# Kernel optimization log

Hardware: AMD Instinct MI355X
Metric: run time of the kernel (lower is better)

## Reference

```python
import jax, jax.numpy as jnp
import numpy as np
from jax import lax

NUM_ROUTES = 3
OUT_CAPS = 8
OUT_CH = 16


def squash(t):
    # squared_norm * t / ((1 + squared_norm) * sqrt(squared_norm)), norm over last dim
    sn = jnp.sum(t * t, axis=-1, keepdims=True)
    return sn * t / ((1.0 + sn) * jnp.sqrt(sn))


def setup_inputs() -> dict:
    key = jax.random.key(0)
    k1, k2 = jax.random.split(key)
    x = jax.random.normal(k1, (16, 8, 16, 128, 128), dtype=jnp.float32)
    # conv weight [out_channels*out_capsules, in_channels, 4, 4], kaiming-ish scale
    W_conv = jax.random.normal(k2, (OUT_CH * OUT_CAPS, 16, 4, 4), dtype=jnp.float32) * 0.05
    b_conv = jnp.zeros((OUT_CH * OUT_CAPS,), dtype=jnp.float32)
    return {"x": x, "W_conv": W_conv, "b_conv": b_conv}


def reference(x, W_conv, b_conv):
    B, IC, Cin, W, H = x.shape
    xr = x.reshape(B * IC, Cin, W, H)
    u = lax.conv_general_dilated(
        xr, W_conv,
        window_strides=(2, 2), padding=((2, 2), (2, 2)),
        dimension_numbers=("NCHW", "OIHW", "NCHW"),
    ) + b_conv[None, :, None, None]
    ow, oh = u.shape[2], u.shape[3]
    # [B*IC, OC*Cout, ow, oh] -> [B, IC, ow, oh, OC, Cout]
    u_hat = u.transpose(0, 2, 3, 1).reshape(B, IC, ow, oh, OUT_CAPS, OUT_CH)

    b_ij = jnp.zeros((1, IC, ow, oh, OUT_CAPS), dtype=u_hat.dtype)
    v_j = None
    for it in range(NUM_ROUTES):
        c_ij = jax.nn.softmax(b_ij, axis=1)[..., None]      # [1,IC,ow,oh,OC,1]
        s_j = jnp.sum(c_ij * u_hat, axis=1)                  # [B,ow,oh,OC,Cout]
        v_j = squash(s_j)
        if it < NUM_ROUTES - 1:
            # agreement: dot over Cout between u_hat and v_j
            a_ij = jnp.einsum('biwhoc,bwhoc->biwho', u_hat, v_j)
            b_ij = b_ij + jnp.mean(a_ij, axis=0, keepdims=True)
    # [B,ow,oh,OC,Cout] -> [B, OC, Cout, ow, oh]
    return v_j.transpose(0, 3, 4, 1, 2)
```

## Files before the change

kernel.cpp:

```cpp
#include <hip/hip_runtime.h>
#include <math.h>

#define BB   16
#define IC   8
#define BI   128
#define CIN  16
#define WH   128
#define OWH  65
#define NPIX (OWH*OWH)
#define OC   8
#define COUT 16
#define NOC  128
#define KTOT 256
#define KC   64
#define NCHUNK 4
#define S_TOTAL (CIN*WH*WH)

#define NCHM 8

typedef unsigned short ushortT;
typedef __bf16 bf16x8 __attribute__((ext_vector_type(8)));
typedef float  f32x4  __attribute__((ext_vector_type(4)));

__device__ __forceinline__ ushortT f2bf(float f) {
    unsigned u = __float_as_uint(f);
    unsigned r = (u + 0x7fffu + ((u >> 16) & 1u)) >> 16;
    return (ushortT)r;
}

template <int CTRL>
__device__ __forceinline__ float dppMov(float x) {
    return __int_as_float(__builtin_amdgcn_update_dpp(
        0, __float_as_int(x), CTRL, 0xF, 0xF, true));
}

#define GEMM_BARRIER() do {                                   \
    asm volatile("s_waitcnt lgkmcnt(0)" ::: "memory");        \
    __builtin_amdgcn_s_barrier();                             \
    __builtin_amdgcn_sched_barrier(0);                        \
} while (0)

__global__ void cvtT_kernel(const float* __restrict__ x,
                            ushortT* __restrict__ xbfT)
{
    __shared__ ushortT tile[64 * 136];
    const int t  = threadIdx.x;
    const int s0 = blockIdx.x * 64;

#pragma unroll
    for (int k = 0; k < 8; ++k) {
        const int j  = t + k * 256;
        const int bi = j >> 4, s4 = j & 15;
        const float4 v = *(const float4*)(x + (size_t)bi * S_TOTAL + s0 + s4 * 4);
        const int si = s4 * 4;
        tile[(si    ) * 136 + (bi ^ (((si    ) & 15) << 3))] = f2bf(v.x);
        tile[(si + 1) * 136 + (bi ^ (((si + 1) & 15) << 3))] = f2bf(v.y);
        tile[(si + 2) * 136 + (bi ^ (((si + 2) & 15) << 3))] = f2bf(v.z);
        tile[(si + 3) * 136 + (bi ^ (((si + 3) & 15) << 3))] = f2bf(v.w);
    }
    __syncthreads();
#pragma unroll
    for (int k = 0; k < 4; ++k) {
        const int j  = t + k * 256;
        const int sI = j >> 4, g = j & 15;
        const uint4 val = *(const uint4*)&tile[sI * 136 + ((g ^ (sI & 15)) << 3)];
        *(uint4*)(xbfT + (size_t)(s0 + sI) * 128 + g * 8) = val;
    }
}

__global__ void prep_w_kernel(const float* __restrict__ W,
                              ushortT* __restrict__ Wbf)
{
    int idx = blockIdx.x * 256 + threadIdx.x;
    int oc = idx >> 8, k = idx & 255;
    int kpg = k >> 3, j = k & 7;
    Wbf[((size_t)kpg * 128 + oc) * 8 + j] = f2bf(W[idx]);
}

__launch_bounds__(512, 4)
__global__ void capsconv_mfma(const ushortT* __restrict__ xbfT,
                              const ushortT* __restrict__ Wbf,
                              const float* __restrict__ bias,
                              float* __restrict__ outbuf,
                              const int direct_out)
{
    __shared__ __align__(16) ushortT As[3][4 * 128 * 8];
    __shared__ float cijs[64];
    __shared__ float bijs[64];
    __shared__ float aTmp[16 * 64];

    const int t  = threadIdx.x;
    const int g8 = blockIdx.x;
    int p = (g8 & 7) * 529 + (g8 >> 3);
    if (p >= NPIX) return;

    const int w  = t >> 6;
    const int ln = t & 63;
    const int q  = ln >> 4;
    const int cL = ln & 15;
    const int h  = q & 1;
    const int mrow_base = 64 * (w >> 2);
    const int ncol_base = 32 * (w & 3);

    const int px = p / OWH;
    const int py = p % OWH;
    const int row0 = 2 * px - 2;
    const int col0 = 2 * py - 2;

    f32x4 acc[4][2];
#pragma unroll
    for (int mt = 0; mt < 4; ++mt)
#pragma unroll
        for (int nt = 0; nt < 2; ++nt) acc[mt][nt] = (f32x4){0.f, 0.f, 0.f, 0.f};

    const int g     = t & 15;
    const int sI    = t >> 4;
    const int colw  = sI & 3;
    const int rowl  = (sI >> 2) & 3;
    const int cih   = sI >> 4;
    const int srow  = row0 + rowl;
    const int scol  = col0 + colw;
    const bool ok   = (srow >= 0 && srow < WH && scol >= 0 && scol < WH);
    const size_t aoff0 = ok
        ? ((size_t)((cih * WH + srow) * WH + scol) * 128 + g * 8)
        : 0;
    const int kpg   = cih * 2 + (rowl >> 1);
    const int jj    = (rowl & 1) * 4 + colw;
    const int wbase = (kpg * 128 + g * 8) * 16 + jj * 2;
    const int gk7   = g & 7;

    int aRd[4];
#pragma unroll
    for (int mt = 0; mt < 4; ++mt) {
        const int by = (q * 128 + mrow_base + mt * 16 + cL) * 16;
        aRd[mt] = by ^ (((by >> 7) & 7) << 4);
    }

    uint4 aR[2];

    auto loadA = [&](uint4& r, int kc) {
        r = make_uint4(0u, 0u, 0u, 0u);
        if (ok) r = *(const uint4*)(xbfT + aoff0 + (size_t)kc * (2 * WH * WH * 128));
    };
    auto storeA = [&](int buf, const uint4& r) {
        char* ab = (char*)&As[buf][0];
        const ushortT* av = (const ushortT*)&r;
#pragma unroll
        for (int c = 0; c < 8; ++c)
            *(ushortT*)(ab + wbase + ((c ^ gk7) << 4)) = av[c];
    };

    loadA(aR[0], 0);
    loadA(aR[1], 1);
    storeA(0, aR[0]);
    loadA(aR[0], 2);
    GEMM_BARRIER();

#pragma unroll
    for (int kc = 0; kc < NCHM; ++kc) {
        const int buf = kc % 3;
        {
            const char* abase = (const char*)&As[buf][0];
            bf16x8 af[4], bfr[2];
#pragma unroll
            for (int mt = 0; mt < 4; ++mt)
                af[mt] = *(const bf16x8*)(abase + aRd[mt]);
            const ushortT* bsrc = Wbf + kc * 4096 + (q * 128 + ncol_base + cL) * 8;
            bfr[0] = *(const bf16x8*)(bsrc);
            bfr[1] = *(const bf16x8*)(bsrc + 128);
#pragma unroll
            for (int mt = 0; mt < 4; ++mt)
#pragma unroll
                for (int nt = 0; nt < 2; ++nt)
                    acc[mt][nt] = __builtin_amdgcn_mfma_f32_16x16x32_bf16(
                        af[mt], bfr[nt], acc[mt][nt], 0, 0, 0);
        }
        if (kc + 1 < NCHM) storeA((kc + 1) % 3, aR[(kc + 1) & 1]);
        if (kc + 3 < NCHM) loadA(aR[(kc + 3) & 1], kc + 3);
        GEMM_BARRIER();
    }

#pragma unroll
    for (int nt = 0; nt < 2; ++nt) {
        const float bv = bias[ncol_base + nt * 16 + cL];
#pragma unroll
        for (int mt = 0; mt < 4; ++mt) acc[mt][nt] += bv;
    }

    for (int it = 0; it < 3; ++it) {
        float4 cf4[2];
        if (it == 0) {
#pragma unroll
            for (int nt = 0; nt < 2; ++nt)
                cf4[nt] = make_float4(0.125f, 0.125f, 0.125f, 0.125f);
        } else {
#pragma unroll
            for (int nt = 0; nt < 2; ++nt)
                cf4[nt] = *(const float4*)&cijs[(2 * (w & 3) + nt) * 8 + 4 * h];
        }

#pragma unroll
        for (int mt = 0; mt < 4; ++mt) {
            const int b = 8 * (w >> 2) + 2 * mt + (q >> 1);
#pragma unroll
            for (int nt = 0; nt < 2; ++nt) {
                const int o = 2 * (w & 3) + nt;
                const float4 cf = cf4[nt];
                float sp = cf.x * acc[mt][nt][0] + cf.y * acc[mt][nt][1]
                         + cf.z * acc[mt][nt][2] + cf.w * acc[mt][nt][3];
                float s = sp + __shfl_xor(sp, 16);
                float ssq = s * s;
                ssq += dppMov<0xB1>(ssq);
                ssq += dppMov<0x4E>(ssq);
                ssq += dppMov<0x124>(ssq);
                ssq += dppMov<0x128>(ssq);
                const float scale = sqrtf(ssq) * __builtin_amdgcn_rcpf(1.f + ssq);
                const float vj = s * scale;

                if (it == 2) {
                    if (q == 0 || q == 2) {
                        if (direct_out)
                            outbuf[(size_t)(b * NOC + o * 16 + cL) * NPIX + p] = vj;
                        else
                            outbuf[(size_t)p * 2048 + b * NOC + o * 16 + cL] = vj;
                    }
                } else {
                    f32x4 ap = acc[mt][nt] * vj;
                    const bool k1 = (cL & 1) != 0;
                    float e0 = k1 ? ap[1] : ap[0];
                    float o0 = k1 ? ap[0] : ap[1];
                    float e1 = k1 ? ap[3] : ap[2];
                    float o1 = k1 ? ap[2] : ap[3];
                    e0 += dppMov<0xB1>(o0);
                    e1 += dppMov<0xB1>(o1);
                    const bool k2 = (cL & 2) != 0;
                    float f0 = k2 ? e1 : e0;
                    float f1 = k2 ? e0 : e1;
                    f0 += dppMov<0x4E>(f1);
                    f0 += dppMov<0x124>(f0);
                    f0 += dppMov<0x128>(f0);
                    if (cL < 4)
                        aTmp[b * 64 + o * 8 + 4 * h + cL] = f0;
                }
            }
        }
        if (it < 2) {
            __syncthreads();
            if (t < 64) {
                float sum = 0.f;
#pragma unroll
                for (int b = 0; b < BB; ++b) sum += aTmp[b * 64 + t];
                float bij = (it == 0 ? 0.f : bijs[t]) + sum * (1.f / 16.f);
                bijs[t] = bij;
                float mx = bij;
                mx = fmaxf(mx, __shfl_xor(mx, 1));
                mx = fmaxf(mx, __shfl_xor(mx, 2));
                mx = fmaxf(mx, __shfl_xor(mx, 4));
                float e = __expf(bij - mx);
                float se = e;
                se += __shfl_xor(se, 1);
                se += __shfl_xor(se, 2);
                se += __shfl_xor(se, 4);
                cijs[t] = e * __builtin_amdgcn_rcpf(se);
            }
            __syncthreads();
        }
    }
}

__global__ void transpose_kernel(const float* __restrict__ vtmp,
                                 float* __restrict__ out)
{
    __shared__ float tile[32][33];
    const int bp = blockIdx.x;
    const int bc = blockIdx.y;
    const int p0 = bp * 32, c0 = bc * 32;
    const int tx = threadIdx.x & 31, ty = threadIdx.x >> 5;

    for (int r = ty; r < 32; r += 8) {
        const int p = p0 + r;
        tile[r][tx] = (p < NPIX) ? vtmp[(size_t)p * 2048 + c0 + tx] : 0.f;
    }
    __syncthreads();
    for (int r = ty; r < 32; r += 8) {
        const int c = c0 + r;
        const int p = p0 + tx;
        if (p < NPIX) out[(size_t)c * NPIX + p] = tile[tx][r];
    }
}

__launch_bounds__(256, 2)
__global__ void capsconv_fp32(const float* __restrict__ x,
                              const float* __restrict__ Wc,
                              const float* __restrict__ bias,
                              float* __restrict__ outbuf,
                              const int direct_out)
{
    __shared__ float As[KC][BI];
    __shared__ float Bsh[KC][NOC];
    __shared__ float cij[64];
    __shared__ float bijs2[64];
    __shared__ float aTmp2[BB * 64];

    const int t  = threadIdx.x;
    const int tn = t & 15;
    const int tm = t >> 4;
    const int p  = blockIdx.x;
    const int px = p / OWH;
    const int py = p % OWH;
    const int row0 = 2 * px - 2;
    const int col0 = 2 * py - 2;
    const bool interior = (px >= 1 && px <= 63 && py >= 1 && py <= 63);

    float C[8][8];
#pragma unroll
    for (int r = 0; r < 8; ++r)
#pragma unroll
        for (int j = 0; j < 8; ++j) C[r][j] = 0.f;

    float areg[8][4];
    float breg[32];

    auto load_chunk = [&](int kc) {
#pragma unroll
        for (int g = 0; g < 8; ++g) {
            const int L    = g * 256 + t;
            const int bi   = L & 127;
            const int cikw = L >> 7;
            const int ci   = kc * 4 + (cikw >> 2);
            const int kw   = cikw & 3;
            const int row  = row0 + kw;
            const float* src = x + (((size_t)(bi * CIN + ci) * WH + row) * WH + col0);
            if (interior) {
                const float2 v01 = *(const float2*)(src);
                const float2 v23 = *(const float2*)(src + 2);
                areg[g][0] = v01.x; areg[g][1] = v01.y;
                areg[g][2] = v23.x; areg[g][3] = v23.y;
            } else {
#pragma unroll
                for (int kh = 0; kh < 4; ++kh) {
                    const int col = col0 + kh;
                    areg[g][kh] = (row >= 0 && row < WH && col >= 0 && col < WH)
                                      ? src[kh] : 0.f;
                }
            }
        }
        {
            const int oc  = t >> 1;
            const int kk0 = (t & 1) * 32;
            const float* wsrc = Wc + (size_t)oc * KTOT + kc * KC + kk0;
#pragma unroll
            for (int m = 0; m < 32; m += 4) {
                const float4 v = *(const float4*)(wsrc + m);
                breg[m] = v.x; breg[m+1] = v.y; breg[m+2] = v.z; breg[m+3] = v.w;
            }
        }
    };

    load_chunk(0);
    for (int kc = 0; kc < NCHUNK; ++kc) {
        __syncthreads();
#pragma unroll
        for (int g = 0; g < 8; ++g) {
            const int L    = g * 256 + t;
            const int bi   = L & 127;
            const int cikw = L >> 7;
            const int kkb  = cikw * 4;
#pragma unroll
            for (int kh = 0; kh < 4; ++kh) As[kkb + kh][bi] = areg[g][kh];
        }
        {
            const int oc  = t >> 1;
            const int kk0 = (t & 1) * 32;
#pragma unroll
            for (int m = 0; m < 32; ++m) Bsh[kk0 + m][oc] = breg[m];
        }
        __syncthreads();
        if (kc < NCHUNK - 1) load_chunk(kc + 1);
#pragma unroll 4
        for (int k = 0; k < KC; ++k) {
            float af[8], bf[8];
            *(float4*)(af)     = *(const float4*)&As[k][tm * 8];
            *(float4*)(af + 4) = *(const float4*)&As[k][tm * 8 + 4];
            *(float4*)(bf)     = *(const float4*)&Bsh[k][tn * 8];
            *(float4*)(bf + 4) = *(const float4*)&Bsh[k][tn * 8 + 4];
#pragma unroll
            for (int r = 0; r < 8; ++r)
#pragma unroll
                for (int j = 0; j < 8; ++j)
                    C[r][j] = fmaf(af[r], bf[j], C[r][j]);
        }
    }
#pragma unroll
    for (int j = 0; j < 8; ++j) {
        const float bj = bias[tn * 8 + j];
#pragma unroll
        for (int r = 0; r < 8; ++r) C[r][j] += bj;
    }

    const int o = tn >> 1;
    __syncthreads();
    if (t < 64) bijs2[t] = 0.f;

    float vout[8];
    for (int it = 0; it < 3; ++it) {
        __syncthreads();
        if (t < 8) {
            const int oo = t;
            float mx = -1e30f;
#pragma unroll
            for (int i = 0; i < 8; ++i) mx = fmaxf(mx, bijs2[i * 8 + oo]);
            float e[8]; float ssum = 0.f;
#pragma unroll
            for (int i = 0; i < 8; ++i) { e[i] = expf(bijs2[i * 8 + oo] - mx); ssum += e[i]; }
            const float inv = 1.f / ssum;
#pragma unroll
            for (int i = 0; i < 8; ++i) cij[i * 8 + oo] = e[i] * inv;
        }
        __syncthreads();
        float cf[8];
#pragma unroll
        for (int i = 0; i < 8; ++i) cf[i] = cij[i * 8 + o];
        float s[8];
#pragma unroll
        for (int j = 0; j < 8; ++j) {
            float acc = 0.f;
#pragma unroll
            for (int r = 0; r < 8; ++r) acc = fmaf(cf[r], C[r][j], acc);
            s[j] = acc;
        }
        float ssq = 0.f;
#pragma unroll
        for (int j = 0; j < 8; ++j) ssq = fmaf(s[j], s[j], ssq);
        ssq += __shfl_xor(ssq, 1);
        const float scale = ssq / ((1.f + ssq) * sqrtf(ssq));
        if (it == 2) {
#pragma unroll
            for (int j = 0; j < 8; ++j) vout[j] = s[j] * scale;
        } else {
            float ap[8];
#pragma unroll
            for (int r = 0; r < 8; ++r) {
                float acc = 0.f;
#pragma unroll
                for (int j = 0; j < 8; ++j) acc = fmaf(C[r][j], s[j] * scale, acc);
                ap[r] = acc;
            }
#pragma unroll
            for (int r = 0; r < 8; ++r) ap[r] += __shfl_xor(ap[r], 1);
            if ((tn & 1) == 0) {
#pragma unroll
                for (int r = 0; r < 8; ++r) aTmp2[tm * 64 + r * 8 + o] = ap[r];
            }
            __syncthreads();
            if (t < 64) {
                float acc = 0.f;
#pragma unroll
                for (int b = 0; b < BB; ++b) acc += aTmp2[b * 64 + t];
                bijs2[t] += acc * (1.f / 16.f);
            }
        }
    }
    if (direct_out) {
#pragma unroll
        for (int j = 0; j < 8; ++j)
            outbuf[(size_t)(tm * NOC + tn * 8 + j) * NPIX + p] = vout[j];
    } else {
        float4* dst = (float4*)(outbuf + (size_t)p * 2048 + tm * NOC + tn * 8);
        dst[0] = make_float4(vout[0], vout[1], vout[2], vout[3]);
        dst[1] = make_float4(vout[4], vout[5], vout[6], vout[7]);
    }
}

extern "C" void kernel_launch(void* const* d_in, const int* in_sizes, int n_in,
                              void* d_out, int out_size, void* d_ws, size_t ws_size,
                              hipStream_t stream)
{
    const float* x    = (const float*)d_in[0];
    const float* Wc   = (const float*)d_in[1];
    const float* bias = (const float*)d_in[2];
    float* out        = (float*)d_out;

    const size_t VT_BYTES = (size_t)NPIX * 2048 * sizeof(float);
    const size_t WB_OFF   = VT_BYTES;
    const size_t XB_OFF   = WB_OFF + 65536;
    const size_t TOTAL    = XB_OFF + (size_t)BI * CIN * WH * WH * 2;

    if (ws_size >= TOTAL) {
        ushortT* Wbf  = (ushortT*)((char*)d_ws + WB_OFF);
        ushortT* xbfT = (ushortT*)((char*)d_ws + XB_OFF);

        cvtT_kernel<<<S_TOTAL / 64, 256, 0, stream>>>(x, xbfT);
        prep_w_kernel<<<128, 256, 0, stream>>>(Wc, Wbf);
        capsconv_mfma<<<529 * 8, 512, 0, stream>>>(xbfT, Wbf, bias, out, 1);
    } else if (ws_size >= VT_BYTES) {
        float* vtmp = (float*)d_ws;
        capsconv_fp32<<<NPIX, 256, 0, stream>>>(x, Wc, bias, vtmp, 0);
        dim3 g((NPIX + 31) / 32, 2048 / 32);
        transpose_kernel<<<g, 256, 0, stream>>>(vtmp, out);
    } else {
        capsconv_fp32<<<NPIX, 256, 0, stream>>>(x, Wc, bias, out, 1);
    }
}
```

Baseline: 336.6 us.

## Process two output pixels per block, prefetching second pixel during routing

Each block now handles two consecutive output pixels: after the first pixel's GEMM, it issues global loads for the second pixel's first three K-chunks before running the first pixel's routing. The intent is to hide global-load latency behind routing math and to halve the block count. The GEMM pipeline is restructured with explicit triple-buffer stores per chunk. Launch bounds are raised to ask for 8 blocks per CU, which may force register spills. Halving the grid may reduce parallelism.

```diff
diff --git a/kernel.cpp b/kernel.cpp
--- a/kernel.cpp
+++ b/kernel.cpp
@@ -34,7 +34,7 @@
         0, __float_as_int(x), CTRL, 0xF, 0xF, true));
 }
 
-#define GEMM_BARRIER() do {                                   \
+#define LDS_BARRIER() do {                                    \
     asm volatile("s_waitcnt lgkmcnt(0)" ::: "memory");        \
     __builtin_amdgcn_s_barrier();                             \
     __builtin_amdgcn_sched_barrier(0);                        \
@@ -77,7 +77,7 @@
     Wbf[((size_t)kpg * 128 + oc) * 8 + j] = f2bf(W[idx]);
 }
 
-__launch_bounds__(512, 4)
+__launch_bounds__(512, 8)
 __global__ void capsconv_mfma(const ushortT* __restrict__ xbfT,
                               const ushortT* __restrict__ Wbf,
                               const float* __restrict__ bias,
@@ -91,8 +91,11 @@
 
     const int t  = threadIdx.x;
     const int g8 = blockIdx.x;
-    int p = (g8 & 7) * 529 + (g8 >> 3);
-    if (p >= NPIX) return;
+    const int strip = g8 & 7;
+    const int jj2   = g8 >> 3;
+    const int p0 = strip * 529 + 2 * jj2;
+    if (p0 >= NPIX) return;
+    const bool p1ok = (2 * jj2 + 1 <= 528) && (p0 + 1 < NPIX);
 
     const int w  = t >> 6;
     const int ln = t & 63;
@@ -102,28 +105,13 @@
     const int mrow_base = 64 * (w >> 2);
     const int ncol_base = 32 * (w & 3);
 
-    const int px = p / OWH;
-    const int py = p % OWH;
-    const int row0 = 2 * px - 2;
-    const int col0 = 2 * py - 2;
-
     f32x4 acc[4][2];
-#pragma unroll
-    for (int mt = 0; mt < 4; ++mt)
-#pragma unroll
-        for (int nt = 0; nt < 2; ++nt) acc[mt][nt] = (f32x4){0.f, 0.f, 0.f, 0.f};
 
     const int g     = t & 15;
     const int sI    = t >> 4;
     const int colw  = sI & 3;
     const int rowl  = (sI >> 2) & 3;
     const int cih   = sI >> 4;
-    const int srow  = row0 + rowl;
-    const int scol  = col0 + colw;
-    const bool ok   = (srow >= 0 && srow < WH && scol >= 0 && scol < WH);
-    const size_t aoff0 = ok
-        ? ((size_t)((cih * WH + srow) * WH + scol) * 128 + g * 8)
-        : 0;
     const int kpg   = cih * 2 + (rowl >> 1);
     const int jj    = (rowl & 1) * 4 + colw;
     const int wbase = (kpg * 128 + g * 8) * 16 + jj * 2;
@@ -136,11 +124,19 @@
         aRd[mt] = by ^ (((by >> 7) & 7) << 4);
     }
 
-    uint4 aR[2];
-
-    auto loadA = [&](uint4& r, int kc) {
+    uint4 aP0, aP1, aP2;
+    uint4 aRr0, aRr1;
+
+    auto mkAddr = [&](int pp, size_t& aoff, bool& okp) {
+        const int ppx = pp / OWH, ppy = pp % OWH;
+        const int srow2 = 2 * ppx - 2 + rowl;
+        const int scol2 = 2 * ppy - 2 + colw;
+        okp = (srow2 >= 0 && srow2 < WH && scol2 >= 0 && scol2 < WH);
+        aoff = okp ? ((size_t)((cih * WH + srow2) * WH + scol2) * 128 + g * 8) : 0;
+    };
+    auto loadAx = [&](uint4& r, int kc, size_t aoff, bool okp) {
         r = make_uint4(0u, 0u, 0u, 0u);
-        if (ok) r = *(const uint4*)(xbfT + aoff0 + (size_t)kc * (2 * WH * WH * 128));
+        if (okp) r = *(const uint4*)(xbfT + aoff + (size_t)kc * (2 * WH * WH * 128));
     };
     auto storeA = [&](int buf, const uint4& r) {
         char* ab = (char*)&As[buf][0];
@@ -149,122 +145,155 @@
         for (int c = 0; c < 8; ++c)
             *(ushortT*)(ab + wbase + ((c ^ gk7) << 4)) = av[c];
     };
-
-    loadA(aR[0], 0);
-    loadA(aR[1], 1);
-    storeA(0, aR[0]);
-    loadA(aR[0], 2);
-    GEMM_BARRIER();
-
-#pragma unroll
-    for (int kc = 0; kc < NCHM; ++kc) {
-        const int buf = kc % 3;
-        {
-            const char* abase = (const char*)&As[buf][0];
-            bf16x8 af[4], bfr[2];
-#pragma unroll
-            for (int mt = 0; mt < 4; ++mt)
-                af[mt] = *(const bf16x8*)(abase + aRd[mt]);
-            const ushortT* bsrc = Wbf + kc * 4096 + (q * 128 + ncol_base + cL) * 8;
-            bfr[0] = *(const bf16x8*)(bsrc);
-            bfr[1] = *(const bf16x8*)(bsrc + 128);
-#pragma unroll
-            for (int mt = 0; mt < 4; ++mt)
+    auto prefetch3 = [&](size_t aoff, bool okp) {
+        loadAx(aP0, 0, aoff, okp);
+        loadAx(aP1, 1, aoff, okp);
+        loadAx(aP2, 2, aoff, okp);
+    };
+
+    auto gemm = [&](size_t aoff, bool okp) {
+#pragma unroll
+        for (int mt = 0; mt < 4; ++mt)
+#pragma unroll
+            for (int nt = 0; nt < 2; ++nt) acc[mt][nt] = (f32x4){0.f, 0.f, 0.f, 0.f};
+
+        loadAx(aRr0, 3, aoff, okp);
+        loadAx(aRr1, 4, aoff, okp);
+        storeA(0, aP0);
+        storeA(1, aP1);
+        storeA(2, aP2);
+        LDS_BARRIER();
+
+#pragma unroll
+        for (int kc = 0; kc < NCHM; ++kc) {
+            {
+                const char* abase = (const char*)&As[kc % 3][0];
+                bf16x8 af[4], bfr[2];
+#pragma unroll
+                for (int mt = 0; mt < 4; ++mt)
+                    af[mt] = *(const bf16x8*)(abase + aRd[mt]);
+                const ushortT* bsrc = Wbf + kc * 4096 + (q * 128 + ncol_base + cL) * 8;
+                bfr[0] = *(const bf16x8*)(bsrc);
+                bfr[1] = *(const bf16x8*)(bsrc + 128);
+#pragma unroll
+                for (int mt = 0; mt < 4; ++mt)
+#pragma unroll
+                    for (int nt = 0; nt < 2; ++nt)
+                        acc[mt][nt] = __builtin_amdgcn_mfma_f32_16x16x32_bf16(
+                            af[mt], bfr[nt], acc[mt][nt], 0, 0, 0);
+            }
+            if (kc == 1)      { storeA(0, aRr0); loadAx(aP0, 5, aoff, okp); }
+            else if (kc == 2) { storeA(1, aRr1); loadAx(aP1, 6, aoff, okp); }
+            else if (kc == 3) { storeA(2, aP0);  loadAx(aP2, 7, aoff, okp); }
+            else if (kc == 4) { storeA(0, aP1); }
+            else if (kc == 5) { storeA(1, aP2); }
+            LDS_BARRIER();
+        }
+
+#pragma unroll
+        for (int nt = 0; nt < 2; ++nt) {
+            const float bv = bias[ncol_base + nt * 16 + cL];
+#pragma unroll
+            for (int mt = 0; mt < 4; ++mt) acc[mt][nt] += bv;
+        }
+    };
+
+    auto routing = [&](int p) {
+        for (int it = 0; it < 3; ++it) {
+            float4 cf4[2];
+            if (it == 0) {
 #pragma unroll
                 for (int nt = 0; nt < 2; ++nt)
-                    acc[mt][nt] = __builtin_amdgcn_mfma_f32_16x16x32_bf16(
-                        af[mt], bfr[nt], acc[mt][nt], 0, 0, 0);
-        }
-        if (kc + 1 < NCHM) storeA((kc + 1) % 3, aR[(kc + 1) & 1]);
-        if (kc + 3 < NCHM) loadA(aR[(kc + 3) & 1], kc + 3);
-        GEMM_BARRIER();
-    }
-
-#pragma unroll
-    for (int nt = 0; nt < 2; ++nt) {
-        const float bv = bias[ncol_base + nt * 16 + cL];
-#pragma unroll
-        for (int mt = 0; mt < 4; ++mt) acc[mt][nt] += bv;
-    }
-
-    for (int it = 0; it < 3; ++it) {
-        float4 cf4[2];
-        if (it == 0) {
-#pragma unroll
-            for (int nt = 0; nt < 2; ++nt)
-                cf4[nt] = make_float4(0.125f, 0.125f, 0.125f, 0.125f);
-        } else {
-#pragma unroll
-            for (int nt = 0; nt < 2; ++nt)
-                cf4[nt] = *(const float4*)&cijs[(2 * (w & 3) + nt) * 8 + 4 * h];
-        }
-
-#pragma unroll
-        for (int mt = 0; mt < 4; ++mt) {
-            const int b = 8 * (w >> 2) + 2 * mt + (q >> 1);
-#pragma unroll
-            for (int nt = 0; nt < 2; ++nt) {
-                const int o = 2 * (w & 3) + nt;
-                const float4 cf = cf4[nt];
-                float sp = cf.x * acc[mt][nt][0] + cf.y * acc[mt][nt][1]
-                         + cf.z * acc[mt][nt][2] + cf.w * acc[mt][nt][3];
-                float s = sp + __shfl_xor(sp, 16);
-                float ssq = s * s;
-                ssq += dppMov<0xB1>(ssq);
-                ssq += dppMov<0x4E>(ssq);
-                ssq += dppMov<0x124>(ssq);
-                ssq += dppMov<0x128>(ssq);
-                const float scale = sqrtf(ssq) * __builtin_amdgcn_rcpf(1.f + ssq);
-                const float vj = s * scale;
-
-                if (it == 2) {
-                    if (q == 0 || q == 2) {
-                        if (direct_out)
-                            outbuf[(size_t)(b * NOC + o * 16 + cL) * NPIX + p] = vj;
-                        else
-                            outbuf[(size_t)p * 2048 + b * NOC + o * 16 + cL] = vj;
+                    cf4[nt] = make_float4(0.125f, 0.125f, 0.125f, 0.125f);
+            } else {
+#pragma unroll
+                for (int nt = 0; nt < 2; ++nt)
+                    cf4[nt] = *(const float4*)&cijs[(2 * (w & 3) + nt) * 8 + 4 * h];
+            }
+
+#pragma unroll
+            for (int mt = 0; mt < 4; ++mt) {
+                const int b = 8 * (w >> 2) + 2 * mt + (q >> 1);
+#pragma unroll
+                for (int nt = 0; nt < 2; ++nt) {
+                    const int o = 2 * (w & 3) + nt;
+                    const float4 cf = cf4[nt];
+                    float sp = cf.x * acc[mt][nt][0] + cf.y * acc[mt][nt][1]
+                             + cf.z * acc[mt][nt][2] + cf.w * acc[mt][nt][3];
+                    float s = sp + __shfl_xor(sp, 16);
+                    float ssq = s * s;
+                    ssq += dppMov<0xB1>(ssq);
+                    ssq += dppMov<0x4E>(ssq);
+                    ssq += dppMov<0x124>(ssq);
+                    ssq += dppMov<0x128>(ssq);
+                    const float scale = sqrtf(ssq) * __builtin_amdgcn_rcpf(1.f + ssq);
+                    const float vj = s * scale;
+
+                    if (it == 2) {
+                        if (q == 0 || q == 2) {
+                            if (direct_out)
+                                outbuf[(size_t)(b * NOC + o * 16 + cL) * NPIX + p] = vj;
+                            else
+                                outbuf[(size_t)p * 2048 + b * NOC + o * 16 + cL] = vj;
+                        }
+                    } else {
+                        f32x4 ap = acc[mt][nt] * vj;
+                        const bool k1 = (cL & 1) != 0;
+                        float e0 = k1 ? ap[1] : ap[0];
+                        float o0 = k1 ? ap[0] : ap[1];
+                        float e1 = k1 ? ap[3] : ap[2];
+                        float o1 = k1 ? ap[2] : ap[3];
+                        e0 += dppMov<0xB1>(o0);
+                        e1 += dppMov<0xB1>(o1);
+                        const bool k2 = (cL & 2) != 0;
+                        float f0 = k2 ? e1 : e0;
+                        float f1 = k2 ? e0 : e1;
+                        f0 += dppMov<0x4E>(f1);
+                        f0 += dppMov<0x124>(f0);
+                        f0 += dppMov<0x128>(f0);
+                        if (cL < 4)
+                            aTmp[b * 64 + o * 8 + 4 * h + cL] = f0;
                     }
-                } else {
-                    f32x4 ap = acc[mt][nt] * vj;
-                    const bool k1 = (cL & 1) != 0;
-                    float e0 = k1 ? ap[1] : ap[0];
-                    float o0 = k1 ? ap[0] : ap[1];
-                    float e1 = k1 ? ap[3] : ap[2];
-                    float o1 = k1 ? ap[2] : ap[3];
-                    e0 += dppMov<0xB1>(o0);
-                    e1 += dppMov<0xB1>(o1);
-                    const bool k2 = (cL & 2) != 0;
-                    float f0 = k2 ? e1 : e0;
-                    float f1 = k2 ? e0 : e1;
-                    f0 += dppMov<0x4E>(f1);
-                    f0 += dppMov<0x124>(f0);
-                    f0 += dppMov<0x128>(f0);
-                    if (cL < 4)
-                        aTmp[b * 64 + o * 8 + 4 * h + cL] = f0;
                 }
             }
-        }
-        if (it < 2) {
-            __syncthreads();
-            if (t < 64) {
-                float sum = 0.f;
-#pragma unroll
-                for (int b = 0; b < BB; ++b) sum += aTmp[b * 64 + t];
-                float bij = (it == 0 ? 0.f : bijs[t]) + sum * (1.f / 16.f);
-                bijs[t] = bij;
-                float mx = bij;
-                mx = fmaxf(mx, __shfl_xor(mx, 1));
-                mx = fmaxf(mx, __shfl_xor(mx, 2));
-                mx = fmaxf(mx, __shfl_xor(mx, 4));
-                float e = __expf(bij - mx);
-                float se = e;
-                se += __shfl_xor(se, 1);
-                se += __shfl_xor(se, 2);
-                se += __shfl_xor(se, 4);
-                cijs[t] = e * __builtin_amdgcn_rcpf(se);
-            }
-            __syncthreads();
-        }
+            if (it < 2) {
+                LDS_BARRIER();
+                if (t < 64) {
+                    float sum = 0.f;
+#pragma unroll
+                    for (int b = 0; b < BB; ++b) sum += aTmp[b * 64 + t];
+                    float bij = (it == 0 ? 0.f : bijs[t]) + sum * (1.f / 16.f);
+                    bijs[t] = bij;
+                    float mx = bij;
+                    mx = fmaxf(mx, __shfl_xor(mx, 1));
+                    mx = fmaxf(mx, __shfl_xor(mx, 2));
+                    mx = fmaxf(mx, __shfl_xor(mx, 4));
+                    float e = __expf(bij - mx);
+                    float se = e;
+                    se += __shfl_xor(se, 1);
+                    se += __shfl_xor(se, 2);
+                    se += __shfl_xor(se, 4);
+                    cijs[t] = e * __builtin_amdgcn_rcpf(se);
+                }
+                LDS_BARRIER();
+            }
+        }
+    };
+
+    size_t aoff0s, aoff1s;
+    bool ok0, ok1;
+    mkAddr(p0, aoff0s, ok0);
+
+    prefetch3(aoff0s, ok0);
+    gemm(aoff0s, ok0);
+    if (p1ok) {
+        mkAddr(p0 + 1, aoff1s, ok1);
+        prefetch3(aoff1s, ok1);
+    }
+    routing(p0);
+    if (p1ok) {
+        gemm(aoff1s, ok1);
+        routing(p0 + 1);
     }
 }
 
@@ -492,7 +521,7 @@
 
         cvtT_kernel<<<S_TOTAL / 64, 256, 0, stream>>>(x, xbfT);
         prep_w_kernel<<<128, 256, 0, stream>>>(Wc, Wbf);
-        capsconv_mfma<<<529 * 8, 512, 0, stream>>>(xbfT, Wbf, bias, out, 1);
+        capsconv_mfma<<<265 * 8, 512, 0, stream>>>(xbfT, Wbf, bias, out, 1);
     } else if (ws_size >= VT_BYTES) {
         float* vtmp = (float*)d_ws;
         capsconv_fp32<<<NPIX, 256, 0, stream>>>(x, Wc, bias, vtmp, 0);
```

Result: slower. 806.5 us (+139.6%).

## Process K chunks in pairs with four LDS buffers and fewer barriers

Applied to the files above, without the earlier changes.

Restructures the conv GEMM main loop so each barrier covers two K chunks, using four LDS A-buffers and four register staging slots with a deeper global-load prefetch. This cuts the number of workgroup barriers from eight to four and issues more loads in flight ahead of use. The routing-phase __syncthreads are also swapped for the lighter LDS-only barrier macro. In exchange it uses more LDS per block and more registers, which could lower occupancy under the 512x4 launch bounds.

```diff
diff --git a/kernel.cpp b/kernel.cpp
--- a/kernel.cpp
+++ b/kernel.cpp
@@ -34,7 +34,7 @@
         0, __float_as_int(x), CTRL, 0xF, 0xF, true));
 }
 
-#define GEMM_BARRIER() do {                                   \
+#define LDS_BARRIER() do {                                    \
     asm volatile("s_waitcnt lgkmcnt(0)" ::: "memory");        \
     __builtin_amdgcn_s_barrier();                             \
     __builtin_amdgcn_sched_barrier(0);                        \
@@ -84,7 +84,7 @@
                               float* __restrict__ outbuf,
                               const int direct_out)
 {
-    __shared__ __align__(16) ushortT As[3][4 * 128 * 8];
+    __shared__ __align__(16) ushortT As[4][4 * 128 * 8];
     __shared__ float cijs[64];
     __shared__ float bijs[64];
     __shared__ float aTmp[16 * 64];
@@ -136,7 +136,7 @@
         aRd[mt] = by ^ (((by >> 7) & 7) << 4);
     }
 
-    uint4 aR[2];
+    uint4 aR0, aR1, aR2, aR3;
 
     auto loadA = [&](uint4& r, int kc) {
         r = make_uint4(0u, 0u, 0u, 0u);
@@ -149,36 +149,43 @@
         for (int c = 0; c < 8; ++c)
             *(ushortT*)(ab + wbase + ((c ^ gk7) << 4)) = av[c];
     };
-
-    loadA(aR[0], 0);
-    loadA(aR[1], 1);
-    storeA(0, aR[0]);
-    loadA(aR[0], 2);
-    GEMM_BARRIER();
-
-#pragma unroll
-    for (int kc = 0; kc < NCHM; ++kc) {
-        const int buf = kc % 3;
-        {
-            const char* abase = (const char*)&As[buf][0];
-            bf16x8 af[4], bfr[2];
-#pragma unroll
-            for (int mt = 0; mt < 4; ++mt)
-                af[mt] = *(const bf16x8*)(abase + aRd[mt]);
-            const ushortT* bsrc = Wbf + kc * 4096 + (q * 128 + ncol_base + cL) * 8;
-            bfr[0] = *(const bf16x8*)(bsrc);
-            bfr[1] = *(const bf16x8*)(bsrc + 128);
-#pragma unroll
-            for (int mt = 0; mt < 4; ++mt)
-#pragma unroll
-                for (int nt = 0; nt < 2; ++nt)
-                    acc[mt][nt] = __builtin_amdgcn_mfma_f32_16x16x32_bf16(
-                        af[mt], bfr[nt], acc[mt][nt], 0, 0, 0);
-        }
-        if (kc + 1 < NCHM) storeA((kc + 1) % 3, aR[(kc + 1) & 1]);
-        if (kc + 3 < NCHM) loadA(aR[(kc + 3) & 1], kc + 3);
-        GEMM_BARRIER();
-    }
+    auto compute = [&](int kc, int buf) {
+        const char* abase = (const char*)&As[buf][0];
+        bf16x8 af[4], bfr[2];
+#pragma unroll
+        for (int mt = 0; mt < 4; ++mt)
+            af[mt] = *(const bf16x8*)(abase + aRd[mt]);
+        const ushortT* bsrc = Wbf + kc * 4096 + (q * 128 + ncol_base + cL) * 8;
+        bfr[0] = *(const bf16x8*)(bsrc);
+        bfr[1] = *(const bf16x8*)(bsrc + 128);
+#pragma unroll
+        for (int mt = 0; mt < 4; ++mt)
+#pragma unroll
+            for (int nt = 0; nt < 2; ++nt)
+                acc[mt][nt] = __builtin_amdgcn_mfma_f32_16x16x32_bf16(
+                    af[mt], bfr[nt], acc[mt][nt], 0, 0, 0);
+    };
+
+    loadA(aR0, 0); loadA(aR1, 1); loadA(aR2, 2); loadA(aR3, 3);
+    storeA(0, aR0);
+    storeA(1, aR1);
+    loadA(aR0, 4); loadA(aR1, 5);
+    LDS_BARRIER();
+
+    compute(0, 0); compute(1, 1);
+    storeA(2, aR2); storeA(3, aR3);
+    loadA(aR2, 6); loadA(aR3, 7);
+    LDS_BARRIER();
+
+    compute(2, 2); compute(3, 3);
+    storeA(0, aR0); storeA(1, aR1);
+    LDS_BARRIER();
+
+    compute(4, 0); compute(5, 1);
+    storeA(2, aR2); storeA(3, aR3);
+    LDS_BARRIER();
+
+    compute(6, 2); compute(7, 3);
 
 #pragma unroll
     for (int nt = 0; nt < 2; ++nt) {
@@ -245,7 +252,7 @@
             }
         }
         if (it < 2) {
-            __syncthreads();
+            LDS_BARRIER();
             if (t < 64) {
                 float sum = 0.f;
 #pragma unroll
@@ -263,7 +270,7 @@
                 se += __shfl_xor(se, 4);
                 cijs[t] = e * __builtin_amdgcn_rcpf(se);
             }
-            __syncthreads();
+            LDS_BARRIER();
         }
     }
 }
```

After: 343.7 us. +2.1%, slower.
